# Optimization experiments

Measured on AMD Instinct MI355X. Metric: run time of the kernel, lower is better.

## Reference

```python
import jax, jax.numpy as jnp
import numpy as np

N, E, F_IN, H, C = 50000, 800000, 256, 64, 40
NEG_SLOPE = 0.2


def setup_inputs() -> dict:
    key = jax.random.key(0)
    ks = jax.random.split(key, 16)
    sc = lambda fan: 1.0 / np.sqrt(fan)
    return {
        "x": jax.random.normal(ks[0], (N, F_IN), dtype=jnp.float32),
        "edge_index": jax.random.randint(ks[1], (2, E), 0, N, dtype=jnp.int64),
        "W1l": jax.random.normal(ks[2], (F_IN, H), dtype=jnp.float32) * sc(F_IN),
        "b1l": jnp.zeros((H,), jnp.float32),
        "W1r": jax.random.normal(ks[3], (F_IN, H), dtype=jnp.float32) * sc(F_IN),
        "b1r": jnp.zeros((H,), jnp.float32),
        "att1": jax.random.normal(ks[4], (H,), dtype=jnp.float32) * sc(H),
        "bias1": jnp.zeros((H,), jnp.float32),
        "lin1_W": jax.random.normal(ks[5], (F_IN, H), dtype=jnp.float32) * sc(F_IN),
        "lin1_b": jnp.zeros((H,), jnp.float32),
        "W2l": jax.random.normal(ks[6], (H, C), dtype=jnp.float32) * sc(H),
        "b2l": jnp.zeros((C,), jnp.float32),
        "W2r": jax.random.normal(ks[7], (H, C), dtype=jnp.float32) * sc(H),
        "b2r": jnp.zeros((C,), jnp.float32),
        "att2": jax.random.normal(ks[8], (C,), dtype=jnp.float32) * sc(C),
        "bias2": jnp.zeros((C,), jnp.float32),
        "lin2_W": jax.random.normal(ks[9], (H, C), dtype=jnp.float32) * sc(H),
        "lin2_b": jnp.zeros((C,), jnp.float32),
    }


def gatv2_layer(x, src, dst, Wl, bl, Wr, br, att, bias, n):
    # PyG GATv2Conv, heads=1: xl = lin_l(x) (source), xr = lin_r(x) (target)
    xl = x @ Wl + bl                               # [n, out]
    xr = x @ Wr + br                               # [n, out]
    m = xl[src] + xr[dst]                          # [E, out] per-edge gather
    e = jax.nn.leaky_relu(m, NEG_SLOPE) @ att      # [E] attention logits
    # segment softmax over destination nodes (self-loops guarantee nonempty segments)
    emax = jax.ops.segment_max(e, dst, num_segments=n)
    ee = jnp.exp(e - emax[dst])
    denom = jax.ops.segment_sum(ee, dst, num_segments=n)
    alpha = ee / denom[dst]                        # [E]
    out = jax.ops.segment_sum(alpha[:, None] * xl[src], dst, num_segments=n)
    return out + bias


def reference(x, edge_index, W1l, b1l, W1r, b1r, att1, bias1, lin1_W, lin1_b,
              W2l, b2l, W2r, b2r, att2, bias2, lin2_W, lin2_b):
    n = x.shape[0]
    loops = jnp.arange(n, dtype=edge_index.dtype)
    src = jnp.concatenate([edge_index[0], loops])  # add_self_loops=True (PyG default)
    dst = jnp.concatenate([edge_index[1], loops])
    h = jax.nn.relu(gatv2_layer(x, src, dst, W1l, b1l, W1r, b1r, att1, bias1, n)
                    + x @ lin1_W + lin1_b)
    o = (gatv2_layer(h, src, dst, W2l, b2l, W2r, b2r, att2, bias2, n)
         + h @ lin2_W + lin2_b)
    return jax.nn.log_softmax(o, axis=1), edge_index
```

## Files before the change

kernel.cpp:

```cpp
#include <hip/hip_runtime.h>
#include <cmath>

#define NN 50000
#define NP 50048
#define NE 800000
#define CD 40
#define NEG_SLOPE 0.2f
#define NITEMS (NE + NN)
#define CHUNK 2048
#define NCH 416
#define NBKT 391
#define BCAP 3072
#define GB1 782
#define TB1 (3 * 64 * 256)
#define TB2 (3 * 64 * 64)
#define WPB 240

typedef __attribute__((ext_vector_type(8))) short s16x8;
typedef __attribute__((ext_vector_type(4))) float f32x4;
typedef __attribute__((ext_vector_type(2))) float f32x2;

__device__ __forceinline__ f32x2 pk_fma(f32x2 a, f32x2 b, f32x2 c) {
#if __has_builtin(__builtin_elementwise_fma)
  return __builtin_elementwise_fma(a, b, c);
#else
  f32x2 r; r[0] = fmaf(a[0], b[0], c[0]); r[1] = fmaf(a[1], b[1], c[1]); return r;
#endif
}
__device__ __forceinline__ f32x2 pk_max(f32x2 a, f32x2 b) {
#if __has_builtin(__builtin_elementwise_max)
  return __builtin_elementwise_max(a, b);
#else
  f32x2 r; r[0] = fmaxf(a[0], b[0]); r[1] = fmaxf(a[1], b[1]); return r;
#endif
}

__device__ __forceinline__ short f2bf(float x) {
  unsigned u = __builtin_bit_cast(unsigned, x);
  u += 0x7fffu + ((u >> 16) & 1u);
  return (short)(u >> 16);
}
__device__ __forceinline__ unsigned pack2(float lo, float hi) {
  return (unsigned)(unsigned short)f2bf(lo) | ((unsigned)(unsigned short)f2bf(hi) << 16);
}
__device__ __forceinline__ float bf2f_lo(unsigned v) {
  return __builtin_bit_cast(float, v << 16);
}
__device__ __forceinline__ float bf2f_hi(unsigned v) {
  return __builtin_bit_cast(float, v & 0xffff0000u);
}
__device__ __forceinline__ void unp8(uint4 v, f32x2* f) {
  f[0] = (f32x2){bf2f_lo(v.x), bf2f_hi(v.x)};
  f[1] = (f32x2){bf2f_lo(v.y), bf2f_hi(v.y)};
  f[2] = (f32x2){bf2f_lo(v.z), bf2f_hi(v.z)};
  f[3] = (f32x2){bf2f_lo(v.w), bf2f_hi(v.w)};
}
__device__ __forceinline__ uint4 zero4() {
  uint4 z; z.x = 0u; z.y = 0u; z.z = 0u; z.w = 0u; return z;
}

__global__ __launch_bounds__(256) void prep_bin(const float* __restrict__ W1l,
                                                const float* __restrict__ W1r,
                                                const float* __restrict__ L1,
                                                const float* __restrict__ W2l,
                                                const float* __restrict__ W2r,
                                                const float* __restrict__ L2,
                                                short* __restrict__ Wp1,
                                                short* __restrict__ Wp2,
                                                const int* __restrict__ ei,
                                                float* __restrict__ outE,
                                                int* __restrict__ gcur,
                                                unsigned* __restrict__ rec) {
  const int tid = threadIdx.x;
  if (blockIdx.x < WPB) {
    int e = blockIdx.x * 256 + tid;
    if (e < TB1) {
      int kb = e / 6144, r = e % 6144;
      int w = r / 2048, r2 = r % 2048;
      int t = r2 / 512, r3 = r2 % 512;
      int lane = r3 / 8, j = r3 % 8;
      int n = t * 16 + (lane & 15);
      int k = kb * 32 + (lane >> 4) * 8 + j;
      const float* W = (w == 0) ? W1l : (w == 1) ? W1r : L1;
      Wp1[e] = f2bf(W[k * 64 + n]);
    } else {
      e -= TB1;
      int kb = e / 6144, r = e % 6144;
      int w = r / 2048, r2 = r % 2048;
      int t = r2 / 512, r3 = r2 % 512;
      int lane = r3 / 8, j = r3 % 8;
      int n = t * 16 + (lane & 15);
      int k = kb * 32 + (lane >> 4) * 8 + j;
      const float* W = (w == 0) ? W2l : (w == 1) ? W2r : L2;
      Wp2[e] = (n < 40) ? f2bf(W[k * 40 + n]) : (short)0;
    }
    return;
  }
  __shared__ unsigned sorted[CHUNK];
  __shared__ int hist[512];
  __shared__ int bcur[512];
  __shared__ int gbase[512];
  const int base = (blockIdx.x - WPB) * CHUNK;
  for (int t = tid; t < 512; t += 256) { hist[t] = 0; bcur[t] = 0; gbase[t] = 0; }
  __syncthreads();
  unsigned key[CHUNK / 256];
#pragma unroll
  for (int u = 0; u < CHUNK / 256; ++u) {
    const int j = base + u * 256 + tid;
    unsigned k = 0xFFFFFFFFu;
    if (j < NITEMS) {
      int s, d;
      if (j < NE) {
        s = ei[j]; d = ei[NE + j];
        outE[j] = (float)s; outE[NE + j] = (float)d;
      } else {
        s = j - NE; d = s;
      }
      k = ((unsigned)d << 16) | (unsigned)s;
      atomicAdd(&hist[k >> 23], 1);
    }
    key[u] = k;
  }
  __syncthreads();
  if (tid < 64) {
    int carry = 0;
#pragma unroll
    for (int c = 0; c < 8; ++c) {
      int v = hist[c * 64 + tid];
      int inc = v;
#pragma unroll
      for (int off = 1; off < 64; off <<= 1) {
        int tt = __shfl_up(inc, off, 64);
        if (tid >= off) inc += tt;
      }
      hist[c * 64 + tid] = carry + inc - v;
      carry += __shfl(inc, 63, 64);
    }
  }
  __syncthreads();
#pragma unroll
  for (int u = 0; u < CHUNK / 256; ++u) {
    const unsigned k = key[u];
    if (k != 0xFFFFFFFFu) {
      const int b = k >> 23;
      sorted[hist[b] + atomicAdd(&bcur[b], 1)] = k;
    }
  }
  __syncthreads();
  for (int t = tid; t < NBKT; t += 256) {
    const int c = bcur[t];
    if (c > 0) gbase[t] = atomicAdd(&gcur[t], c);
  }
  __syncthreads();
  const int cnt = min(CHUNK, NITEMS - base);
  for (int i = tid; i < cnt; i += 256) {
    const unsigned k = sorted[i];
    const int b = k >> 23;
    const int p = gbase[b] + (i - hist[b]);
    if (p < BCAP) rec[(size_t)b * BCAP + p] = k;
  }
}

__device__ __forceinline__ void gemm1_body(int bid, const float* __restrict__ X,
                                           const short* __restrict__ Wp,
                                           const float* __restrict__ B0,
                                           const float* __restrict__ B1,
                                           const float* __restrict__ B2,
                                           unsigned short* __restrict__ Y0,
                                           unsigned short* __restrict__ Y1,
                                           unsigned short* __restrict__ Y2) {
  const int lane = threadIdx.x & 63;
  const int wave = threadIdx.x >> 6;
  const int r0 = bid * 64 + wave * 16;
  const int m = lane & 15;
  const int q = lane >> 4;
  f32x4 acc[3][4] = {};
  const float* a0 = X + (size_t)min(r0 + m, NN - 1) * 256 + q * 8;
  const short* bp = Wp + lane * 8;
  float4 v0 = *reinterpret_cast<const float4*>(a0);
  float4 v1 = *reinterpret_cast<const float4*>(a0 + 4);
#pragma unroll
  for (int kb = 0; kb < 8; ++kb) {
    s16x8 bf[12];
#pragma unroll
    for (int i = 0; i < 12; ++i)
      bf[i] = *reinterpret_cast<const s16x8*>(bp + (size_t)(kb * 12 + i) * 512);
    s16x8 af;
    af[0] = f2bf(v0.x); af[1] = f2bf(v0.y); af[2] = f2bf(v0.z); af[3] = f2bf(v0.w);
    af[4] = f2bf(v1.x); af[5] = f2bf(v1.y); af[6] = f2bf(v1.z); af[7] = f2bf(v1.w);
    if (kb < 7) {
      v0 = *reinterpret_cast<const float4*>(a0 + (kb + 1) * 32);
      v1 = *reinterpret_cast<const float4*>(a0 + (kb + 1) * 32 + 4);
    }
#pragma unroll
    for (int i = 0; i < 12; ++i)
      acc[i >> 2][i & 3] = __builtin_amdgcn_mfma_f32_16x16x32_bf16(
          af, bf[i], acc[i >> 2][i & 3], 0, 0, 0);
  }
#pragma unroll
  for (int w = 0; w < 3; ++w) {
    const float* B = (w == 0) ? B0 : (w == 1) ? B1 : B2;
    unsigned short* Y = (w == 0) ? Y0 : (w == 1) ? Y1 : Y2;
#pragma unroll
    for (int t = 0; t < 4; ++t) {
      const int c = t * 16 + m;
      const float bv = B[c];
#pragma unroll
      for (int rg = 0; rg < 4; ++rg) {
        const int row = r0 + q * 4 + rg;
        if (row < NN)
          Y[(size_t)row * 64 + c] = (unsigned short)f2bf(acc[w][t][rg] + bv);
      }
    }
  }
}

__global__ __launch_bounds__(256, 2) void build_gemm1(
    const float* __restrict__ X, const short* __restrict__ Wp1,
    const float* __restrict__ B0, const float* __restrict__ B1,
    const float* __restrict__ B2, unsigned short* __restrict__ Y0,
    unsigned short* __restrict__ Y1, unsigned short* __restrict__ Y2,
    const int* __restrict__ gcur, const unsigned* __restrict__ rec,
    int* __restrict__ offsets, unsigned short* __restrict__ csr16) {
  if (blockIdx.x < GB1) {
    gemm1_body(blockIdx.x, X, Wp1, B0, B1, B2, Y0, Y1, Y2);
    return;
  }
  const int b = blockIdx.x - GB1;
  const int tid = threadIdx.x;
  __shared__ unsigned recs[BCAP];
  __shared__ int red[256];
  __shared__ int cnt[128];
  __shared__ int sc[128];
  __shared__ int cur[128];
  int acc = 0;
  for (int t = tid; t < NBKT; t += 256)
    if (t < b) acc += gcur[t];
  red[tid] = acc;
  __syncthreads();
#pragma unroll
  for (int off = 128; off >= 1; off >>= 1) {
    if (tid < off) red[tid] += red[tid + off];
    __syncthreads();
  }
  const int base = red[0];
  const int Tb = min(gcur[b], BCAP);
  if (tid < 128) cnt[tid] = 0;
  __syncthreads();
  for (int i = tid; i < Tb; i += 256) {
    const unsigned k = rec[(size_t)b * BCAP + i];
    recs[i] = k;
    atomicAdd(&cnt[(k >> 16) & 127], 1);
  }
  __syncthreads();
  if (tid < 128) sc[tid] = cnt[tid];
  __syncthreads();
#pragma unroll
  for (int off = 1; off < 128; off <<= 1) {
    int v = (tid < 128 && tid >= off) ? sc[tid - off] : 0;
    __syncthreads();
    if (tid < 128) sc[tid] += v;
    __syncthreads();
  }
  if (tid < 128) {
    const int n = b * 128 + tid;
    if (n < NN) offsets[n + 1] = base + sc[tid];
    cur[tid] = sc[tid] - cnt[tid];
  }
  if (b == 0 && tid == 0) offsets[0] = 0;
  __syncthreads();
  for (int i = tid; i < Tb; i += 256) {
    const unsigned k = recs[i];
    const int p = atomicAdd(&cur[(k >> 16) & 127], 1);
    csr16[base + p] = (unsigned short)(k & 0xFFFFu);
  }
}

__global__ __launch_bounds__(256, 2) void gemm2(const short* __restrict__ Xb,
                                                const short* __restrict__ Wp,
                                                const float* __restrict__ B0,
                                                const float* __restrict__ B1,
                                                const float* __restrict__ B2,
                                                unsigned short* __restrict__ Y0,
                                                unsigned short* __restrict__ Y1,
                                                unsigned short* __restrict__ Y2) {
  const int lane = threadIdx.x & 63;
  const int wave = threadIdx.x >> 6;
  const int r0 = blockIdx.x * 64 + wave * 16;
  const int m = lane & 15;
  const int q = lane >> 4;
  f32x4 acc[3][3] = {};
  const short* a0 = Xb + (size_t)(r0 + m) * 64 + q * 8;
  const short* bp = Wp + lane * 8;
#pragma unroll
  for (int kb = 0; kb < 2; ++kb) {
    s16x8 bf[9];
#pragma unroll
    for (int w = 0; w < 3; ++w)
#pragma unroll
      for (int t = 0; t < 3; ++t)
        bf[w * 3 + t] =
            *reinterpret_cast<const s16x8*>(bp + (size_t)(kb * 12 + w * 4 + t) * 512);
    const s16x8 af = *reinterpret_cast<const s16x8*>(a0 + kb * 32);
#pragma unroll
    for (int w = 0; w < 3; ++w)
#pragma unroll
      for (int t = 0; t < 3; ++t)
        acc[w][t] = __builtin_amdgcn_mfma_f32_16x16x32_bf16(af, bf[w * 3 + t],
                                                            acc[w][t], 0, 0, 0);
  }
#pragma unroll
  for (int w = 0; w < 3; ++w) {
    const float* B = (w == 0) ? B0 : (w == 1) ? B1 : B2;
    unsigned short* Y = (w == 0) ? Y0 : (w == 1) ? Y1 : Y2;
#pragma unroll
    for (int t = 0; t < 3; ++t) {
      const int c = t * 16 + m;
      if (c < 40) {
        const float bv = B[c];
#pragma unroll
        for (int rg = 0; rg < 4; ++rg) {
          const int row = r0 + q * 4 + rg;
          if (row < NN)
            Y[(size_t)row * 64 + c] = (unsigned short)f2bf(acc[w][t][rg] + bv);
        }
      }
    }
  }
}

template <int OC, bool FINAL>
__global__ __launch_bounds__(256) void gat_agg(const unsigned short* __restrict__ XL,
                                               const unsigned short* __restrict__ XR,
                                               const unsigned short* __restrict__ XLIN,
                                               const float* __restrict__ att,
                                               const float* __restrict__ bias,
                                               const int* __restrict__ offsets,
                                               const unsigned short* __restrict__ csr,
                                               float* __restrict__ out,
                                               unsigned short* __restrict__ outb) {
  const int lane = threadIdx.x & 63;
  const int g = lane >> 3;
  const int l = lane & 7;
  const int d = blockIdx.x * 4 + (threadIdx.x >> 6);
  if (d >= NN) return;
  constexpr bool FULLW = (OC >= 64);
  const bool dimok = FULLW || (8 * l < OC);
  const int beg = offsets[d];
  const int end = offsets[d + 1];
  f32x2 a2[4] = {};
  if (dimok) {
    const float4 t0 = *reinterpret_cast<const float4*>(&att[8 * l]);
    const float4 t1 = *reinterpret_cast<const float4*>(&att[8 * l + 4]);
    a2[0] = (f32x2){t0.x, t0.y}; a2[1] = (f32x2){t0.z, t0.w};
    a2[2] = (f32x2){t1.x, t1.y}; a2[3] = (f32x2){t1.z, t1.w};
  }
  f32x2 xr2[4];
  unp8(dimok ? *reinterpret_cast<const uint4*>(XR + (size_t)d * 64 + 8 * l) : zero4(),
       xr2);
  const uint4 xlin_raw =
      dimok ? *reinterpret_cast<const uint4*>(XLIN + (size_t)d * 64 + 8 * l) : zero4();
  float D = 0.f;
  f32x2 A2[4] = {};
  const f32x2 ns = (f32x2){NEG_SLOPE, NEG_SLOPE};
  const int nit = (end - beg + 7) >> 3;
  int idx = beg + g;
  int sa = (int)csr[(idx < end) ? idx : beg];
  uint4 rn0 = dimok ? *reinterpret_cast<const uint4*>(XL + (size_t)sa * 64 + 8 * l)
                    : zero4();
  idx += 8;
  sa = (int)csr[(idx < end) ? idx : beg];
  uint4 rn1 = dimok ? *reinterpret_cast<const uint4*>(XL + (size_t)sa * 64 + 8 * l)
                    : zero4();
  idx += 8;
  sa = (int)csr[(idx < end) ? idx : beg];
  for (int it = 0; it < nit; ++it) {
    const uint4 raw = rn0;
    rn0 = rn1;
    rn1 = dimok ? *reinterpret_cast<const uint4*>(XL + (size_t)sa * 64 + 8 * l)
                : zero4();
    idx += 8;
    sa = (int)csr[(idx < end) ? idx : beg];
    const bool act = (beg + it * 8 + g) < end;
    f32x2 xl2[4];
    unp8(raw, xl2);
    f32x2 pacc = (f32x2){0.f, 0.f};
#pragma unroll
    for (int j = 0; j < 4; ++j) {
      const f32x2 t = xl2[j] + xr2[j];
      const f32x2 lr = pk_max(t, t * ns);
      pacc = pk_fma(lr, a2[j], pacc);
    }
    float p = pacc[0] + pacc[1];
    p += __shfl_xor(p, 1, 64);
    p += __shfl_xor(p, 2, 64);
    p += __shfl_xor(p, 4, 64);
    const float w = __expf(act ? p : -INFINITY);
    D += w;
    const f32x2 w2 = (f32x2){w, w};
#pragma unroll
    for (int j = 0; j < 4; ++j) A2[j] = pk_fma(w2, xl2[j], A2[j]);
  }
  D += __shfl_xor(D, 8, 64);
  D += __shfl_xor(D, 16, 64);
  D += __shfl_xor(D, 32, 64);
  float A[8];
#pragma unroll
  for (int j = 0; j < 4; ++j) {
#pragma unroll
    for (int c = 0; c < 2; ++c) {
      float v = A2[j][c];
      v += __shfl_xor(v, 8, 64);
      v += __shfl_xor(v, 16, 64);
      v += __shfl_xor(v, 32, 64);
      A[j * 2 + c] = v;
    }
  }
  f32x2 xlin2[4];
  unp8(xlin_raw, xlin2);
  float b[8] = {};
  if (dimok) {
    const float4 t0 = *reinterpret_cast<const float4*>(&bias[8 * l]);
    const float4 t1 = *reinterpret_cast<const float4*>(&bias[8 * l + 4]);
    b[0] = t0.x; b[1] = t0.y; b[2] = t0.z; b[3] = t0.w;
    b[4] = t1.x; b[5] = t1.y; b[6] = t1.z; b[7] = t1.w;
  }
  const float inv = 1.0f / D;
  float val[8];
#pragma unroll
  for (int j = 0; j < 8; ++j)
    val[j] = fmaf(A[j], inv, b[j]) + xlin2[j >> 1][j & 1];
  if (!FINAL) {
    if (g == 0) {
      uint4 o;
      o.x = pack2(fmaxf(val[0], 0.f), fmaxf(val[1], 0.f));
      o.y = pack2(fmaxf(val[2], 0.f), fmaxf(val[3], 0.f));
      o.z = pack2(fmaxf(val[4], 0.f), fmaxf(val[5], 0.f));
      o.w = pack2(fmaxf(val[6], 0.f), fmaxf(val[7], 0.f));
      *reinterpret_cast<uint4*>(&outb[(size_t)d * 64 + 8 * l]) = o;
    }
  } else {
    float mx = -3e38f;
    if (dimok) {
#pragma unroll
      for (int j = 0; j < 8; ++j) mx = fmaxf(mx, val[j]);
    }
    mx = fmaxf(mx, __shfl_xor(mx, 1, 64));
    mx = fmaxf(mx, __shfl_xor(mx, 2, 64));
    mx = fmaxf(mx, __shfl_xor(mx, 4, 64));
    float es = 0.f;
    if (dimok) {
#pragma unroll
      for (int j = 0; j < 8; ++j) es += __expf(val[j] - mx);
    }
    es += __shfl_xor(es, 1, 64);
    es += __shfl_xor(es, 2, 64);
    es += __shfl_xor(es, 4, 64);
    const float lse = mx + __logf(es);
    if (g == 0 && dimok) {
      float4 o0, o1;
      o0.x = val[0] - lse; o0.y = val[1] - lse; o0.z = val[2] - lse; o0.w = val[3] - lse;
      o1.x = val[4] - lse; o1.y = val[5] - lse; o1.z = val[6] - lse; o1.w = val[7] - lse;
      float* dst = &out[(size_t)d * OC + 8 * l];
      *reinterpret_cast<float4*>(dst) = o0;
      *reinterpret_cast<float4*>(dst + 4) = o1;
    }
  }
}

extern "C" void kernel_launch(void* const* d_in, const int* in_sizes, int n_in,
                              void* d_out, int out_size, void* d_ws, size_t ws_size,
                              hipStream_t stream) {
  const float* x     = (const float*)d_in[0];
  const int*   ei    = (const int*)d_in[1];
  const float* W1l   = (const float*)d_in[2];
  const float* b1l   = (const float*)d_in[3];
  const float* W1r   = (const float*)d_in[4];
  const float* b1r   = (const float*)d_in[5];
  const float* att1  = (const float*)d_in[6];
  const float* bias1 = (const float*)d_in[7];
  const float* lin1W = (const float*)d_in[8];
  const float* lin1b = (const float*)d_in[9];
  const float* W2l   = (const float*)d_in[10];
  const float* b2l   = (const float*)d_in[11];
  const float* W2r   = (const float*)d_in[12];
  const float* b2r   = (const float*)d_in[13];
  const float* att2  = (const float*)d_in[14];
  const float* bias2 = (const float*)d_in[15];
  const float* lin2W = (const float*)d_in[16];
  const float* lin2b = (const float*)d_in[17];
  float* out = (float*)d_out;

  char* ws = (char*)d_ws;
  size_t off = 0;
  auto alloc = [&](size_t bytes) -> void* {
    void* p = ws + off;
    off += (bytes + 255) & ~(size_t)255;
    return p;
  };
  short* Wp1 = (short*)alloc((size_t)TB1 * 2);
  short* Wp2 = (short*)alloc((size_t)TB2 * 2);
  unsigned short* XL1   = (unsigned short*)alloc((size_t)NN * 64 * 2);
  unsigned short* XR1   = (unsigned short*)alloc((size_t)NN * 64 * 2);
  unsigned short* XLIN1 = (unsigned short*)alloc((size_t)NN * 64 * 2);
  unsigned short* Hb    = (unsigned short*)alloc((size_t)NP * 64 * 2);
  unsigned short* XL2   = (unsigned short*)alloc((size_t)NN * 64 * 2);
  unsigned short* XR2   = (unsigned short*)alloc((size_t)NN * 64 * 2);
  unsigned short* XLIN2 = (unsigned short*)alloc((size_t)NN * 64 * 2);
  int* gcur    = (int*)alloc((size_t)NBKT * 4);
  int* offsets = (int*)alloc((size_t)(NN + 1) * 4);
  unsigned* rec = (unsigned*)alloc((size_t)NBKT * BCAP * 4);
  unsigned short* csr = (unsigned short*)alloc((size_t)NITEMS * 2);

  hipMemsetAsync(gcur, 0, (size_t)NBKT * 4, stream);
  prep_bin<<<WPB + NCH, 256, 0, stream>>>(W1l, W1r, lin1W, W2l, W2r, lin2W,
                                          Wp1, Wp2, ei, out + (size_t)NN * CD,
                                          gcur, rec);
  build_gemm1<<<GB1 + NBKT, 256, 0, stream>>>(x, Wp1, b1l, b1r, lin1b,
                                              XL1, XR1, XLIN1, gcur, rec,
                                              offsets, csr);
  gat_agg<64, false><<<(NN + 3) / 4, 256, 0, stream>>>(XL1, XR1, XLIN1, att1,
                                                       bias1, offsets, csr,
                                                       nullptr, Hb);
  gemm2<<<GB1, 256, 0, stream>>>((const short*)Hb, Wp2, b2l, b2r, lin2b,
                                 XL2, XR2, XLIN2);
  gat_agg<40, true><<<(NN + 3) / 4, 256, 0, stream>>>(XL2, XR2, XLIN2, att2,
                                                      bias2, offsets, csr,
                                                      out, nullptr);
}
```

Before: 245.9 us.

## Map eight destination nodes per wavefront in GAT aggregation instead of one

Each wavefront now handles 8 destination nodes, one per 8-lane group, instead of spreading one node's edges across the 8 groups. The loop runs to the maximum degree among the 8 nodes and masks inactive iterations. This removes the cross-group shuffle reductions and lets every group write its own output. The cost is divergence, since groups whose node has a low degree sit idle while the group with the highest degree finishes. The prefetch depth also drops from two rows to one, which may expose more gather latency.

```diff
diff --git a/kernel.cpp b/kernel.cpp
--- a/kernel.cpp
+++ b/kernel.cpp
@@ -342,12 +342,21 @@
   const int lane = threadIdx.x & 63;
   const int g = lane >> 3;
   const int l = lane & 7;
-  const int d = blockIdx.x * 4 + (threadIdx.x >> 6);
-  if (d >= NN) return;
+  const int wv = threadIdx.x >> 6;
+  const int d = (blockIdx.x * 4 + wv) * 8 + g;
+  const int dd = min(d, NN - 1);
   constexpr bool FULLW = (OC >= 64);
   const bool dimok = FULLW || (8 * l < OC);
-  const int beg = offsets[d];
-  const int end = offsets[d + 1];
+
+  const int beg = offsets[dd];
+  int end = offsets[dd + 1];
+  if (d >= NN) end = beg;
+  const int deg = end - beg;
+  int mdeg = deg;
+  mdeg = max(mdeg, __shfl_xor(mdeg, 8, 64));
+  mdeg = max(mdeg, __shfl_xor(mdeg, 16, 64));
+  mdeg = max(mdeg, __shfl_xor(mdeg, 32, 64));
+
   f32x2 a2[4] = {};
   if (dimok) {
     const float4 t0 = *reinterpret_cast<const float4*>(&att[8 * l]);
@@ -356,32 +365,21 @@
     a2[2] = (f32x2){t1.x, t1.y}; a2[3] = (f32x2){t1.z, t1.w};
   }
   f32x2 xr2[4];
-  unp8(dimok ? *reinterpret_cast<const uint4*>(XR + (size_t)d * 64 + 8 * l) : zero4(),
+  unp8(dimok ? *reinterpret_cast<const uint4*>(XR + (size_t)dd * 64 + 8 * l) : zero4(),
        xr2);
-  const uint4 xlin_raw =
-      dimok ? *reinterpret_cast<const uint4*>(XLIN + (size_t)d * 64 + 8 * l) : zero4();
+
+  const unsigned short* XLl = XL + 8 * l;
   float D = 0.f;
   f32x2 A2[4] = {};
   const f32x2 ns = (f32x2){NEG_SLOPE, NEG_SLOPE};
-  const int nit = (end - beg + 7) >> 3;
-  int idx = beg + g;
-  int sa = (int)csr[(idx < end) ? idx : beg];
-  uint4 rn0 = dimok ? *reinterpret_cast<const uint4*>(XL + (size_t)sa * 64 + 8 * l)
-                    : zero4();
-  idx += 8;
-  sa = (int)csr[(idx < end) ? idx : beg];
-  uint4 rn1 = dimok ? *reinterpret_cast<const uint4*>(XL + (size_t)sa * 64 + 8 * l)
-                    : zero4();
-  idx += 8;
-  sa = (int)csr[(idx < end) ? idx : beg];
-  for (int it = 0; it < nit; ++it) {
-    const uint4 raw = rn0;
-    rn0 = rn1;
-    rn1 = dimok ? *reinterpret_cast<const uint4*>(XL + (size_t)sa * 64 + 8 * l)
-                : zero4();
-    idx += 8;
-    sa = (int)csr[(idx < end) ? idx : beg];
-    const bool act = (beg + it * 8 + g) < end;
+  const int CL = NITEMS - 1;
+  int sa = (int)csr[min(beg, CL)];
+  uint4 rn = dimok ? *reinterpret_cast<const uint4*>(XLl + (size_t)sa * 64) : zero4();
+  sa = (int)csr[min(beg + 1, CL)];
+  for (int it = 0; it < mdeg; ++it) {
+    const uint4 raw = rn;
+    rn = dimok ? *reinterpret_cast<const uint4*>(XLl + (size_t)sa * 64) : zero4();
+    sa = (int)csr[min(beg + it + 2, CL)];
     f32x2 xl2[4];
     unp8(raw, xl2);
     f32x2 pacc = (f32x2){0.f, 0.f};
@@ -395,29 +393,17 @@
     p += __shfl_xor(p, 1, 64);
     p += __shfl_xor(p, 2, 64);
     p += __shfl_xor(p, 4, 64);
-    const float w = __expf(act ? p : -INFINITY);
+    const float w = (it < deg) ? __expf(p) : 0.f;
     D += w;
     const f32x2 w2 = (f32x2){w, w};
 #pragma unroll
     for (int j = 0; j < 4; ++j) A2[j] = pk_fma(w2, xl2[j], A2[j]);
   }
-  D += __shfl_xor(D, 8, 64);
-  D += __shfl_xor(D, 16, 64);
-  D += __shfl_xor(D, 32, 64);
-  float A[8];
-#pragma unroll
-  for (int j = 0; j < 4; ++j) {
-#pragma unroll
-    for (int c = 0; c < 2; ++c) {
-      float v = A2[j][c];
-      v += __shfl_xor(v, 8, 64);
-      v += __shfl_xor(v, 16, 64);
-      v += __shfl_xor(v, 32, 64);
-      A[j * 2 + c] = v;
-    }
-  }
+  if (d >= NN) return;
   f32x2 xlin2[4];
-  unp8(xlin_raw, xlin2);
+  unp8(dimok ? *reinterpret_cast<const uint4*>(XLIN + (size_t)dd * 64 + 8 * l)
+             : zero4(),
+       xlin2);
   float b[8] = {};
   if (dimok) {
     const float4 t0 = *reinterpret_cast<const float4*>(&bias[8 * l]);
@@ -429,16 +415,14 @@
   float val[8];
 #pragma unroll
   for (int j = 0; j < 8; ++j)
-    val[j] = fmaf(A[j], inv, b[j]) + xlin2[j >> 1][j & 1];
+    val[j] = fmaf(A2[j >> 1][j & 1], inv, b[j]) + xlin2[j >> 1][j & 1];
   if (!FINAL) {
-    if (g == 0) {
-      uint4 o;
-      o.x = pack2(fmaxf(val[0], 0.f), fmaxf(val[1], 0.f));
-      o.y = pack2(fmaxf(val[2], 0.f), fmaxf(val[3], 0.f));
-      o.z = pack2(fmaxf(val[4], 0.f), fmaxf(val[5], 0.f));
-      o.w = pack2(fmaxf(val[6], 0.f), fmaxf(val[7], 0.f));
-      *reinterpret_cast<uint4*>(&outb[(size_t)d * 64 + 8 * l]) = o;
-    }
+    uint4 o;
+    o.x = pack2(fmaxf(val[0], 0.f), fmaxf(val[1], 0.f));
+    o.y = pack2(fmaxf(val[2], 0.f), fmaxf(val[3], 0.f));
+    o.z = pack2(fmaxf(val[4], 0.f), fmaxf(val[5], 0.f));
+    o.w = pack2(fmaxf(val[6], 0.f), fmaxf(val[7], 0.f));
+    *reinterpret_cast<uint4*>(&outb[(size_t)d * 64 + 8 * l]) = o;
   } else {
     float mx = -3e38f;
     if (dimok) {
@@ -457,7 +441,7 @@
     es += __shfl_xor(es, 2, 64);
     es += __shfl_xor(es, 4, 64);
     const float lse = mx + __logf(es);
-    if (g == 0 && dimok) {
+    if (dimok) {
       float4 o0, o1;
       o0.x = val[0] - lse; o0.y = val[1] - lse; o0.z = val[2] - lse; o0.w = val[3] - lse;
       o1.x = val[4] - lse; o1.y = val[5] - lse; o1.z = val[6] - lse; o1.w = val[7] - lse;
@@ -519,12 +503,13 @@
   build_gemm1<<<GB1 + NBKT, 256, 0, stream>>>(x, Wp1, b1l, b1r, lin1b,
                                               XL1, XR1, XLIN1, gcur, rec,
                                               offsets, csr);
-  gat_agg<64, false><<<(NN + 3) / 4, 256, 0, stream>>>(XL1, XR1, XLIN1, att1,
-                                                       bias1, offsets, csr,
-                                                       nullptr, Hb);
+  const int AGG_BLOCKS = (NN + 31) / 32;
+  gat_agg<64, false><<<AGG_BLOCKS, 256, 0, stream>>>(XL1, XR1, XLIN1, att1,
+                                                     bias1, offsets, csr,
+                                                     nullptr, Hb);
   gemm2<<<GB1, 256, 0, stream>>>((const short*)Hb, Wp2, b2l, b2r, lin2b,
                                  XL2, XR2, XLIN2);
-  gat_agg<40, true><<<(NN + 3) / 4, 256, 0, stream>>>(XL2, XR2, XLIN2, att2,
-                                                      bias2, offsets, csr,
-                                                      out, nullptr);
-}
+  gat_agg<40, true><<<AGG_BLOCKS, 256, 0, stream>>>(XL2, XR2, XLIN2, att2,
+                                                    bias2, offsets, csr,
+                                                    out, nullptr);
+}
```

New measurement: 232.5 us. -5.5%, faster.
